# Kernel tuning notes

Measured on AMD Instinct MI355X. Metric: run time of the kernel, lower is better.

The kernel has to match this reference:

```python
import jax, jax.numpy as jnp
import numpy as np

N_QUBITS = 4

def _apply_shared(state, U, q, n):
    # apply 2x2 gate U (shared across batch) to qubit q; axis n-q of state holds qubit q
    ax = n - q
    s = jnp.moveaxis(state, ax, -1)
    s = jnp.einsum('b...i,ji->b...j', s, U)
    return jnp.moveaxis(s, -1, ax)

def _apply_batched(state, U, q, n):
    # per-sample 2x2 gates U: [B,2,2]
    ax = n - q
    s = jnp.moveaxis(state, ax, -1)
    s = jnp.einsum('b...i,bji->b...j', s, U)
    return jnp.moveaxis(s, -1, ax)

def _cx(state, c, t, n):
    # CNOT: flip target bit where control bit == 1
    axc, axt = n - c, n - t
    c0 = jnp.take(state, jnp.array([0]), axis=axc)
    c1 = jnp.take(state, jnp.array([1]), axis=axc)
    c1 = jnp.flip(c1, axis=axt)
    return jnp.concatenate([c0, c1], axis=axc)

def _simulate(angles, theta, n=N_QUBITS):
    # batched 4-qubit statevector simulation of the fixed variational circuit
    B = angles.shape[0]
    state = jnp.zeros((B, 2 ** n), jnp.complex64).at[:, 0].set(1.0).reshape((B,) + (2,) * n)
    # data-encoding RY rotations (per-sample angles)
    for q in range(n):
        th = angles[:, q]
        c = jnp.cos(th / 2).astype(jnp.complex64)
        s = jnp.sin(th / 2).astype(jnp.complex64)
        U = jnp.stack([jnp.stack([c, -s], -1), jnp.stack([s, c], -1)], -2)  # [B,2,2]
        state = _apply_batched(state, U, q, n)
    # two variational layers: RX,RY,RZ (same angle) per qubit, then CX chain + wrap-around CX
    for layer in range(2):
        for q in range(n):
            th = theta[layer * n + q]
            c = jnp.cos(th / 2).astype(jnp.complex64)
            s = jnp.sin(th / 2).astype(jnp.complex64)
            Urx = jnp.stack([jnp.stack([c, -1j * s]), jnp.stack([-1j * s, c])])
            Ury = jnp.stack([jnp.stack([c, -s]), jnp.stack([s, c])])
            Urz = jnp.diag(jnp.stack([jnp.exp(-0.5j * th), jnp.exp(0.5j * th)])).astype(jnp.complex64)
            for U in (Urx, Ury, Urz):
                state = _apply_shared(state, U, q, n)
        for q in range(n - 1):
            state = _cx(state, q, q + 1, n)
        if n > 2:
            state = _cx(state, n - 1, 0, n)
    probs = jnp.abs(state) ** 2  # [B,2,2,2,2]; axis n-q corresponds to qubit q
    feats = []
    for i in range(n):
        # Qiskit Pauli label ordering: feature i is <Z_{n-1-i}>
        q = n - 1 - i
        ax = n - q
        other = tuple(a for a in range(1, n + 1) if a != ax)
        m = probs.sum(axis=other)  # [B,2]
        feats.append(m[:, 0] - m[:, 1])
    return jnp.stack(feats, axis=1).astype(jnp.float32)  # [B, n]

def setup_inputs() -> dict:
    key = jax.random.key(0)
    ks = jax.random.split(key, 8)
    B, D, L, n = 32768, 1024, 64, N_QUBITS
    return {
        'x': jax.random.normal(ks[0], (B, D), jnp.float32),
        'W1': jax.random.normal(ks[1], (2 * n, D), jnp.float32) / np.sqrt(D).astype(np.float32),
        'b1': jax.random.normal(ks[2], (2 * n,), jnp.float32) * 0.01,
        'quantum_params': jax.random.normal(ks[3], (3 * n,), jnp.float32) * 0.1,
        'W_mu': jax.random.normal(ks[4], (L, n), jnp.float32) / np.sqrt(n).astype(np.float32),
        'b_mu': jax.random.normal(ks[5], (L,), jnp.float32) * 0.01,
        'W_lv': jax.random.normal(ks[6], (L, n), jnp.float32) / np.sqrt(n).astype(np.float32),
        'b_lv': jax.random.normal(ks[7], (L,), jnp.float32) * 0.01,
    }

def reference(x, W1, b1, quantum_params, W_mu, b_mu, W_lv, b_lv):
    co = jnp.tanh(x @ W1.T + b1)            # [B, 2n]
    angles = co[:, :N_QUBITS]               # only first n_qubits used as RY angles
    # original detaches inputs to the quantum circuit -> no grad flows through it
    qf = jax.lax.stop_gradient(_simulate(angles, quantum_params))  # [B, n]
    mu = qf @ W_mu.T + b_mu
    logvar = qf @ W_lv.T + b_lv
    return (mu, logvar)
```

## Files before the change

### kernel.cpp

```cpp
#include <hip/hip_runtime.h>

typedef float f32x4 __attribute__((ext_vector_type(4)));

#define D_IN 1024

__device__ __forceinline__ float fast_tanh(float x) {
  float e = __expf(2.0f * x);
  return 1.0f - 2.0f * __builtin_amdgcn_rcpf(e + 1.0f);
}

__global__ __launch_bounds__(256) void dots_kernel(
    const float* __restrict__ x, const float* __restrict__ W1,
    float* __restrict__ dots, int B) {
  __shared__ f32x4 W1L[1024];

  const int tid = threadIdx.x;
  {
    const f32x4* wp = reinterpret_cast<const f32x4*>(W1);
#pragma unroll
    for (int k = 0; k < 4; ++k) W1L[k * 256 + tid] = wp[k * 256 + tid];
  }
  __syncthreads();

  const int lane = tid & 63;
  const int p = lane & 3;
  const int wave = blockIdx.x * 4 + (tid >> 6);
  const int row = wave * 16 + (lane >> 2);
  if (row >= B) return;

  const float* xr = x + (size_t)row * D_IN;
  float acc[4] = {0.f, 0.f, 0.f, 0.f};

#pragma unroll
  for (int g = 0; g < 16; ++g) {
    const int db = g * 64 + p * 16;
    f32x4 xv[4];
#pragma unroll
    for (int k = 0; k < 4; ++k)
      xv[k] = *reinterpret_cast<const f32x4*>(xr + db + 4 * k);
#pragma unroll
    for (int k = 0; k < 4; ++k) {
      const int wi = (db >> 2) + k;
      f32x4 xk = xv[k];
#pragma unroll
      for (int j = 0; j < 4; ++j) {
        f32x4 w = W1L[j * 256 + wi];
        acc[j] = fmaf(xk.x, w.x, acc[j]);
        acc[j] = fmaf(xk.y, w.y, acc[j]);
        acc[j] = fmaf(xk.z, w.z, acc[j]);
        acc[j] = fmaf(xk.w, w.w, acc[j]);
      }
    }
  }

#pragma unroll
  for (int j = 0; j < 4; ++j) {
    acc[j] += __shfl_xor(acc[j], 1);
    acc[j] += __shfl_xor(acc[j], 2);
  }
  float outv = (p == 0) ? acc[0] : (p == 1) ? acc[1] : (p == 2) ? acc[2] : acc[3];
  dots[(size_t)row * 4 + p] = outv;
}

__global__ __launch_bounds__(256) void tail_kernel(
    const float* __restrict__ dots, const float* __restrict__ b1,
    const float* __restrict__ theta,
    const float* __restrict__ Wmu, const float* __restrict__ bmu,
    const float* __restrict__ Wlv, const float* __restrict__ blv,
    float* __restrict__ out, int B) {
  __shared__ float Vre[16][17];
  __shared__ float Vim[16][17];
  __shared__ float Mlds[4][16][16];

  const int tid = threadIdx.x;

  if (tid < 16) {
    float re[16], im[16];
#pragma unroll
    for (int z = 0; z < 16; ++z) { re[z] = 0.f; im[z] = 0.f; }
    re[tid] = 1.f;
    for (int layer = 0; layer < 2; ++layer) {
#pragma unroll
      for (int q = 0; q < 4; ++q) {
        float th = theta[layer * 4 + q];
        float s, c;
        __sincosf(0.5f * th, &s, &c);
#pragma unroll
        for (int z = 0; z < 16; ++z) {
          if (!((z >> q) & 1)) {
            int z1 = z | (1 << q);
            float ar = re[z], ai = im[z], br = re[z1], bi = im[z1];
            re[z]  = c * ar + s * bi;  im[z]  = c * ai - s * br;
            re[z1] = c * br + s * ai;  im[z1] = c * bi - s * ar;
          }
        }
#pragma unroll
        for (int z = 0; z < 16; ++z) {
          if (!((z >> q) & 1)) {
            int z1 = z | (1 << q);
            float ar = re[z], ai = im[z], br = re[z1], bi = im[z1];
            re[z]  = c * ar - s * br;  im[z]  = c * ai - s * bi;
            re[z1] = s * ar + c * br;  im[z1] = s * ai + c * bi;
          }
        }
#pragma unroll
        for (int z = 0; z < 16; ++z) {
          if (!((z >> q) & 1)) {
            int z1 = z | (1 << q);
            float ar = re[z], ai = im[z], br = re[z1], bi = im[z1];
            re[z]  = c * ar + s * ai;  im[z]  = c * ai - s * ar;
            re[z1] = c * br - s * bi;  im[z1] = c * bi + s * br;
          }
        }
      }
      const int cqs[4] = {0, 1, 2, 3};
      const int tqs[4] = {1, 2, 3, 0};
#pragma unroll
      for (int gIdx = 0; gIdx < 4; ++gIdx) {
#pragma unroll
        for (int z = 0; z < 16; ++z) {
          if (((z >> cqs[gIdx]) & 1) && !((z >> tqs[gIdx]) & 1)) {
            int z1 = z | (1 << tqs[gIdx]);
            float tr = re[z], ti = im[z];
            re[z] = re[z1];  im[z] = im[z1];
            re[z1] = tr;     im[z1] = ti;
          }
        }
      }
    }
#pragma unroll
    for (int z = 0; z < 16; ++z) { Vre[z][tid] = re[z]; Vim[z][tid] = im[z]; }
  }
  __syncthreads();

  {
    const int i = tid >> 6, a = (tid >> 2) & 15, b0 = (tid & 3) * 4;
    float ra[16], ia[16];
#pragma unroll
    for (int z = 0; z < 16; ++z) { ra[z] = Vre[z][a]; ia[z] = Vim[z][a]; }
#pragma unroll
    for (int k = 0; k < 4; ++k) {
      const int b = b0 + k;
      float acc = 0.f;
#pragma unroll
      for (int z = 0; z < 16; ++z) {
        float sg = ((z >> (3 - i)) & 1) ? -1.f : 1.f;
        acc += sg * (ra[z] * Vre[z][b] + ia[z] * Vim[z][b]);
      }
      Mlds[i][a][b] = acc;
    }
  }
  __syncthreads();

  const int lane = tid & 63;
  const int wave = blockIdx.x * 4 + (tid >> 6);
  const int nwaves = gridDim.x * 4;
  const int g = lane >> 4;
  const int mz = lane & 15;

  float Mr[16];
#pragma unroll
  for (int k = 0; k < 16; ++k) Mr[k] = Mlds[g][mz][k];

  float b1r[4];
#pragma unroll
  for (int j = 0; j < 4; ++j) b1r[j] = b1[j];

  float wmuP[4], wlvP[4];
#pragma unroll
  for (int k = 0; k < 4; ++k) {
    wmuP[k] = Wmu[lane * 4 + (g ^ k)];
    wlvP[k] = Wlv[lane * 4 + (g ^ k)];
  }
  const float bmur = bmu[lane], blvr = blv[lane];
  const size_t lv_base = (size_t)B * 64;

  for (int r = wave; r < B; r += nwaves) {
    const float4 dv = *reinterpret_cast<const float4*>(dots + (size_t)r * 4);

    float cq[4], sq[4];
    __sincosf(0.5f * fast_tanh(dv.x + b1r[0]), &sq[0], &cq[0]);
    __sincosf(0.5f * fast_tanh(dv.y + b1r[1]), &sq[1], &cq[1]);
    __sincosf(0.5f * fast_tanh(dv.z + b1r[2]), &sq[2], &cq[2]);
    __sincosf(0.5f * fast_tanh(dv.w + b1r[3]), &sq[3], &cq[3]);

    const float A0 = cq[0] * cq[1], A1 = sq[0] * cq[1];
    const float A2 = cq[0] * sq[1], A3 = sq[0] * sq[1];
    const float B0 = cq[2] * cq[3], B1 = sq[2] * cq[3];
    const float B2 = cq[2] * sq[3], B3 = sq[2] * sq[3];

    float t0 = fmaf(Mr[3], A3, fmaf(Mr[2], A2, fmaf(Mr[1], A1, Mr[0] * A0)));
    float t1 = fmaf(Mr[7], A3, fmaf(Mr[6], A2, fmaf(Mr[5], A1, Mr[4] * A0)));
    float t2 = fmaf(Mr[11], A3, fmaf(Mr[10], A2, fmaf(Mr[9], A1, Mr[8] * A0)));
    float t3 = fmaf(Mr[15], A3, fmaf(Mr[14], A2, fmaf(Mr[13], A1, Mr[12] * A0)));
    float tdot = fmaf(t3, B3, fmaf(t2, B2, fmaf(t1, B1, t0 * B0)));

    float svm = ((mz & 1) ? sq[0] : cq[0]);
    svm *= ((mz & 2) ? sq[1] : cq[1]);
    svm *= ((mz & 4) ? sq[2] : cq[2]);
    svm *= ((mz & 8) ? sq[3] : cq[3]);

    float pacc = tdot * svm;
#pragma unroll
    for (int off = 8; off; off >>= 1) pacc += __shfl_xor(pacc, off);
    float v1 = __shfl_xor(pacc, 16);
    float v2 = __shfl_xor(pacc, 32);
    float v3 = __shfl_xor(v1, 32);

    float mu = fmaf(v3, wmuP[3], fmaf(v2, wmuP[2], fmaf(v1, wmuP[1], fmaf(pacc, wmuP[0], bmur))));
    float lv = fmaf(v3, wlvP[3], fmaf(v2, wlvP[2], fmaf(v1, wlvP[1], fmaf(pacc, wlvP[0], blvr))));
    __builtin_nontemporal_store(mu, out + (size_t)r * 64 + lane);
    __builtin_nontemporal_store(lv, out + lv_base + (size_t)r * 64 + lane);
  }
}

extern "C" void kernel_launch(void* const* d_in, const int* in_sizes, int n_in,
                              void* d_out, int out_size, void* d_ws, size_t ws_size,
                              hipStream_t stream) {
  const float* x   = (const float*)d_in[0];
  const float* W1  = (const float*)d_in[1];
  const float* b1  = (const float*)d_in[2];
  const float* qp  = (const float*)d_in[3];
  const float* Wmu = (const float*)d_in[4];
  const float* bmu = (const float*)d_in[5];
  const float* Wlv = (const float*)d_in[6];
  const float* blv = (const float*)d_in[7];
  float* out = (float*)d_out;
  float* dots = (float*)d_ws;

  const int B = out_size / 128;

  int blocks1 = (B + 63) / 64;
  dots_kernel<<<blocks1, 256, 0, stream>>>(x, W1, dots, B);

  int blocks2 = (B + 31) / 32;
  if (blocks2 > 1024) blocks2 = 1024;
  tail_kernel<<<blocks2, 256, 0, stream>>>(dots, b1, qp, Wmu, bmu, Wlv, blv,
                                           out, B);
}
```

Measured before the change: 40.99 us.

## Map one row per wave with coalesced loads, prefetch, and grid-stride loop

The x·W1ᵀ dot kernel now gives each wave one whole row, with lanes reading contiguous float4 chunks, instead of 16 rows per wave with 4 lanes per row. Waves loop over rows in grid-stride fashion and load the next row's x before reducing the current one, overlapping memory with compute. The grid is capped at 2048 blocks so the W1 copy into LDS is paid by fewer blocks. In exchange, the cross-lane reduction now needs a full 64-lane butterfly per row instead of two shuffles.

```diff
diff --git a/kernel.cpp b/kernel.cpp
--- a/kernel.cpp
+++ b/kernel.cpp
@@ -23,43 +23,58 @@
   __syncthreads();
 
   const int lane = tid & 63;
-  const int p = lane & 3;
   const int wave = blockIdx.x * 4 + (tid >> 6);
-  const int row = wave * 16 + (lane >> 2);
-  if (row >= B) return;
-
-  const float* xr = x + (size_t)row * D_IN;
-  float acc[4] = {0.f, 0.f, 0.f, 0.f};
-
-#pragma unroll
-  for (int g = 0; g < 16; ++g) {
-    const int db = g * 64 + p * 16;
-    f32x4 xv[4];
-#pragma unroll
-    for (int k = 0; k < 4; ++k)
-      xv[k] = *reinterpret_cast<const f32x4*>(xr + db + 4 * k);
+  const int nwaves = gridDim.x * 4;
+  const bool bit4 = (lane & 16) != 0;
+  const bool bit5 = (lane & 32) != 0;
+  const int f = 2 * (int)bit4 + (int)bit5;
+
+  int r = wave;
+  if (r >= B) return;
+
+  f32x4 xv[4];
+  {
+    const f32x4* xp = reinterpret_cast<const f32x4*>(x + (size_t)r * D_IN);
+#pragma unroll
+    for (int k = 0; k < 4; ++k) xv[k] = xp[k * 64 + lane];
+  }
+
+  while (true) {
+    float acc[4] = {0.f, 0.f, 0.f, 0.f};
 #pragma unroll
     for (int k = 0; k < 4; ++k) {
-      const int wi = (db >> 2) + k;
       f32x4 xk = xv[k];
 #pragma unroll
       for (int j = 0; j < 4; ++j) {
-        f32x4 w = W1L[j * 256 + wi];
+        f32x4 w = W1L[j * 256 + k * 64 + lane];
         acc[j] = fmaf(xk.x, w.x, acc[j]);
         acc[j] = fmaf(xk.y, w.y, acc[j]);
         acc[j] = fmaf(xk.z, w.z, acc[j]);
         acc[j] = fmaf(xk.w, w.w, acc[j]);
       }
     }
-  }
-
-#pragma unroll
-  for (int j = 0; j < 4; ++j) {
-    acc[j] += __shfl_xor(acc[j], 1);
-    acc[j] += __shfl_xor(acc[j], 2);
-  }
-  float outv = (p == 0) ? acc[0] : (p == 1) ? acc[1] : (p == 2) ? acc[2] : acc[3];
-  dots[(size_t)row * 4 + p] = outv;
+
+    const int rn = r + nwaves;
+    if (rn < B) {
+      const f32x4* xp = reinterpret_cast<const f32x4*>(x + (size_t)rn * D_IN);
+#pragma unroll
+      for (int k = 0; k < 4; ++k) xv[k] = xp[k * 64 + lane];
+    }
+
+    float u = bit5 ? acc[1] : acc[0];
+    u += __shfl_xor(bit5 ? acc[0] : acc[1], 32);
+    float v = bit5 ? acc[3] : acc[2];
+    v += __shfl_xor(bit5 ? acc[2] : acc[3], 32);
+    float w = bit4 ? v : u;
+    w += __shfl_xor(bit4 ? u : v, 16);
+#pragma unroll
+    for (int off = 8; off; off >>= 1) w += __shfl_xor(w, off);
+
+    if ((lane & 15) == 0) dots[(size_t)r * 4 + f] = w;
+
+    if (rn >= B) break;
+    r = rn;
+  }
 }
 
 __global__ __launch_bounds__(256) void tail_kernel(
@@ -230,7 +245,8 @@
 
   const int B = out_size / 128;
 
-  int blocks1 = (B + 63) / 64;
+  int blocks1 = (B + 3) / 4;
+  if (blocks1 > 2048) blocks1 = 2048;
   dots_kernel<<<blocks1, 256, 0, stream>>>(x, W1, dots, B);
 
   int blocks2 = (B + 31) / 32;
```

Result: slower. 43.31 us (+5.7%).
